# Performance work log

Hardware: AMD Instinct MI355X
Metric: run time of the kernel (lower is better)

## Reference

```python
import jax, jax.numpy as jnp
import numpy as np

EPS = 1e-5  # torch BatchNorm2d default eps

def _bn(x, gamma, beta):
    # training-mode batch statistics over (N,H,W), per channel (biased variance)
    mean = jnp.mean(x, axis=(0, 2, 3), keepdims=True)
    var = jnp.var(x, axis=(0, 2, 3), keepdims=True)
    return gamma[None, :, None, None] * (x - mean) * jax.lax.rsqrt(var + EPS) + beta[None, :, None, None]

def _conv1x1(x, w, b):
    # (B,C,H,W) x (O,C) -> (B,O,H,W)
    return jnp.einsum('bchw,oc->bohw', x, w) + b[None, :, None, None]

def _maxpool2(x):
    B, C, H, W = x.shape
    return x.reshape(B, C, H // 2, 2, W // 2, 2).max(axis=(3, 5))

def setup_inputs() -> dict:
    key = jax.random.key(0)
    ks = jax.random.split(key, 5)
    B, C, H, W = 16, 256, 56, 56
    Ci, Cg = C // 8, C // 4
    def kaiming(k, o, i):
        return jax.random.normal(k, (o, i), jnp.float32) * np.float32(np.sqrt(2.0 / i))
    return {
        'x': jax.random.normal(ks[0], (B, C, H, W), jnp.float32),
        'bn1_gamma': jnp.ones((C,), jnp.float32),
        'bn1_beta': jnp.zeros((C,), jnp.float32),
        'w_g': kaiming(ks[1], Cg, C), 'b_g': jnp.zeros((Cg,), jnp.float32),
        'w_theta': kaiming(ks[2], Ci, C), 'b_theta': jnp.zeros((Ci,), jnp.float32),
        'w_phi': kaiming(ks[3], Ci, C), 'b_phi': jnp.zeros((Ci,), jnp.float32),
        'bn2_gamma': jnp.ones((Cg,), jnp.float32),
        'bn2_beta': jnp.zeros((Cg,), jnp.float32),
        'w_z': kaiming(ks[4], C, Cg), 'b_z': jnp.zeros((C,), jnp.float32),
    }

def reference(x, bn1_gamma, bn1_beta, w_g, b_g, w_theta, b_theta, w_phi, b_phi, bn2_gamma, bn2_beta, w_z, b_z):
    identity = x
    B, C, H, W = x.shape
    xa = jax.nn.relu(_bn(x, bn1_gamma, bn1_beta))
    g_x = _maxpool2(_conv1x1(xa, w_g, b_g))        # (B,Cg,H/2,W/2)
    phi_x = _maxpool2(_conv1x1(xa, w_phi, b_phi))  # (B,Ci,H/2,W/2)
    theta_x = _conv1x1(xa, w_theta, b_theta)       # (B,Ci,H,W)
    Cg = g_x.shape[1]
    Ci = theta_x.shape[1]
    Np = g_x.shape[2] * g_x.shape[3]               # subsampled positions (H/2*W/2)
    g_x = g_x.reshape(B, Cg, Np).transpose(0, 2, 1)      # (B,Np,Cg)
    phi_x = phi_x.reshape(B, Ci, Np)                     # (B,Ci,Np)
    theta_x = theta_x.reshape(B, Ci, H * W).transpose(0, 2, 1)  # (B,HW,Ci)
    f_div_C = jnp.einsum('bnc,bcm->bnm', theta_x, phi_x) / Np   # (B,HW,Np)
    y = jnp.einsum('bnm,bmc->bnc', f_div_C, g_x)                # (B,HW,Cg)
    y = y.transpose(0, 2, 1).reshape(B, Cg, H, W)
    w_y = _conv1x1(jax.nn.relu(_bn(y, bn2_gamma, bn2_beta)), w_z, b_z)
    return w_y + identity
```

## Files before the change

### kernel.cpp

```cpp
#include <hip/hip_runtime.h>
#include <hip/hip_bf16.h>

#define BB 16
#define CC 256
#define HWN 3136
#define NCG 64
#define NCI 32
#define NPP 784

typedef __attribute__((ext_vector_type(8))) short short8;
typedef __attribute__((ext_vector_type(4))) float floatx4;

__device__ __forceinline__ unsigned short f2bf(float f) {
    union { __hip_bfloat16 h; unsigned short u; } cv;
    cv.h = __float2bfloat16(f);
    return cv.u;
}
__device__ __forceinline__ float bf2f(unsigned short u) {
    return __uint_as_float(((unsigned)u) << 16);
}

__global__ __launch_bounds__(256) void k_head(const float* __restrict__ x,
                                              const float* __restrict__ w_t,
                                              const float* __restrict__ w_p,
                                              const float* __restrict__ w_g,
                                              const float* __restrict__ w_z,
                                              unsigned short* __restrict__ wcat,
                                              unsigned short* __restrict__ wzb,
                                              unsigned short* __restrict__ pool,
                                              float* __restrict__ zacc,
                                              float* __restrict__ bn1part) {
    int blk = blockIdx.x;
    int c = threadIdx.x;
    if (blk < 128) {
        int o = blk;
        const float* src = (o < 32) ? (w_t + o * CC)
                          : (o < 64) ? (w_p + (o - 32) * CC)
                                     : (w_g + (o - 64) * CC);
        wcat[o * CC + c] = f2bf(src[c]);
        {
            int r = o * 2 + (c >> 7);
            int kk = c & 127;
            if (kk < 72)
                wzb[r * 72 + kk] = (kk < 64) ? f2bf(w_z[r * 64 + kk]) : (unsigned short)0;
        }
        if (o < 96) {
            int b = c >> 4, kk = c & 15;
            pool[((size_t)(b * 96 + o)) * 800 + 784 + kk] = 0;
        }
        int idx = o * 256 + c;
        if (idx < 17024) zacc[idx] = 0.f;
        return;
    }
    int bc = blk - 128;
    const float4* p = (const float4*)(x + (size_t)bc * HWN);
    int tid = c;
    float s = 0.f, q = 0.f;
    for (int i = tid; i < 784; i += 256) {
        float4 v = p[i];
        s += v.x + v.y + v.z + v.w;
        q += v.x * v.x + v.y * v.y + v.z * v.z + v.w * v.w;
    }
    #pragma unroll
    for (int off = 32; off > 0; off >>= 1) {
        s += __shfl_down(s, off);
        q += __shfl_down(q, off);
    }
    __shared__ float sh[16];
    int wid = tid >> 6, lane = tid & 63;
    if (lane == 0) { sh[wid] = s; sh[8 + wid] = q; }
    __syncthreads();
    if (tid == 0) bn1part[bc]        = sh[0] + sh[1] + sh[2] + sh[3];
    if (tid == 1) bn1part[4096 + bc] = sh[8] + sh[9] + sh[10] + sh[11];
}

__global__ __launch_bounds__(256) void k_conv1(const float* __restrict__ x,
                                               const unsigned short* __restrict__ wcat,
                                               const float* __restrict__ bn1part,
                                               const float* __restrict__ gamma,
                                               const float* __restrict__ beta,
                                               const float* __restrict__ b_g,
                                               const float* __restrict__ b_t,
                                               const float* __restrict__ b_p,
                                               unsigned short* __restrict__ th,
                                               unsigned short* __restrict__ pool,
                                               float* __restrict__ T1g,
                                               float* __restrict__ Gg) {
    int b  = blockIdx.y;
    int bx = blockIdx.x;
    int hw0 = bx * 112;
    int tid = threadIdx.x;
    int wv = tid >> 6, ln = tid & 63;
    int col = ln & 15, quad = ln >> 4;

    __shared__ unsigned short smem[128 * 120];
    unsigned short* As = smem;
    unsigned short* Bs = smem + 4096;
    __shared__ float ab_s[512];
    __shared__ float bias_s[128];

    {
        const float inv = 1.0f / (BB * HWN);
        float s = 0.f, q = 0.f;
        #pragma unroll
        for (int b2 = 0; b2 < BB; ++b2) {
            s += bn1part[b2 * 256 + tid];
            q += bn1part[4096 + b2 * 256 + tid];
        }
        float mean = s * inv;
        float var  = q * inv - mean * mean;
        float a = gamma[tid] * rsqrtf(var + 1e-5f);
        ab_s[tid] = a;
        ab_s[CC + tid] = beta[tid] - mean * a;
    }
    if (tid < 128) {
        int o = tid;
        bias_s[o] = (o < 32) ? b_t[o] : (o < 64) ? b_p[o - 32] : b_g[o - 64];
    }
    __syncthreads();

    floatx4 acc[2][7];
    #pragma unroll
    for (int mt = 0; mt < 2; ++mt)
        for (int nt = 0; nt < 7; ++nt)
            acc[mt][nt] = (floatx4){0.f, 0.f, 0.f, 0.f};

    int p   = tid & 15;
    int hwq = tid >> 4;
    const float* xb = x + (size_t)(b * CC) * HWN + hw0;
    bool q1 = (hwq + 16) < 28;

    float4 pv0[2], pv1[2];
    {
        int c0 = 2 * p;
        pv0[0] = *(const float4*)(xb + (size_t)c0 * HWN + hwq * 4);
        pv1[0] = *(const float4*)(xb + (size_t)(c0 + 1) * HWN + hwq * 4);
        if (q1) {
            pv0[1] = *(const float4*)(xb + (size_t)c0 * HWN + (hwq + 16) * 4);
            pv1[1] = *(const float4*)(xb + (size_t)(c0 + 1) * HWN + (hwq + 16) * 4);
        }
    }

    for (int k0 = 0; k0 < CC; k0 += 32) {
        #pragma unroll
        for (int i = 0; i < 2; ++i) {
            int row = wv * 32 + i * 16 + (ln >> 2);
            int q   = ln & 3;
            const unsigned short* gp = wcat + row * CC + k0 + q * 8;
            __builtin_amdgcn_global_load_lds(
                (const __attribute__((address_space(1))) unsigned int*)gp,
                (__attribute__((address_space(3))) unsigned int*)&As[(wv * 2 + i) * 512],
                16, 0, 0);
        }
        {
            int c0 = k0 + 2 * p;
            float a0 = ab_s[c0],     d0 = ab_s[CC + c0];
            float a1 = ab_s[c0 + 1], d1 = ab_s[CC + c0 + 1];
            unsigned int* bw = (unsigned int*)Bs;
            #pragma unroll
            for (int t = 0; t < 2; ++t) {
                if (t == 0 || q1) {
                    int qi = hwq + 16 * t;
                    float4 v0 = pv0[t], v1 = pv1[t];
                    float r0[4] = { fmaxf(fmaf(a0, v0.x, d0), 0.f), fmaxf(fmaf(a0, v0.y, d0), 0.f),
                                    fmaxf(fmaf(a0, v0.z, d0), 0.f), fmaxf(fmaf(a0, v0.w, d0), 0.f) };
                    float r1[4] = { fmaxf(fmaf(a1, v1.x, d1), 0.f), fmaxf(fmaf(a1, v1.y, d1), 0.f),
                                    fmaxf(fmaf(a1, v1.z, d1), 0.f), fmaxf(fmaf(a1, v1.w, d1), 0.f) };
                    #pragma unroll
                    for (int i = 0; i < 4; ++i) {
                        unsigned int w = (unsigned int)f2bf(r0[i]) | ((unsigned int)f2bf(r1[i]) << 16);
                        bw[(qi * 4 + i) * 16 + p] = w;
                    }
                }
            }
        }
        __syncthreads();

        if (k0 + 32 < CC) {
            int c0 = k0 + 32 + 2 * p;
            pv0[0] = *(const float4*)(xb + (size_t)c0 * HWN + hwq * 4);
            pv1[0] = *(const float4*)(xb + (size_t)(c0 + 1) * HWN + hwq * 4);
            if (q1) {
                pv0[1] = *(const float4*)(xb + (size_t)c0 * HWN + (hwq + 16) * 4);
                pv1[1] = *(const float4*)(xb + (size_t)(c0 + 1) * HWN + (hwq + 16) * 4);
            }
        }

        short8 af0 = *(const short8*)&As[(wv * 32 +      col) * 32 + quad * 8];
        short8 af1 = *(const short8*)&As[(wv * 32 + 16 + col) * 32 + quad * 8];
        #pragma unroll
        for (int nt = 0; nt < 7; ++nt) {
            short8 bf = *(const short8*)&Bs[(nt * 16 + col) * 32 + quad * 8];
            acc[0][nt] = __builtin_amdgcn_mfma_f32_16x16x32_bf16(af0, bf, acc[0][nt], 0, 0, 0);
            acc[1][nt] = __builtin_amdgcn_mfma_f32_16x16x32_bf16(af1, bf, acc[1][nt], 0, 0, 0);
        }
        __syncthreads();
    }

    unsigned short* Ct = smem;
    #pragma unroll
    for (int mt = 0; mt < 2; ++mt) {
        int obase = wv * 32 + mt * 16 + quad * 4;
        #pragma unroll
        for (int r = 0; r < 4; ++r) {
            float bias = bias_s[obase + r];
            #pragma unroll
            for (int nt = 0; nt < 7; ++nt)
                Ct[(obase + r) * 120 + nt * 16 + col] = f2bf(acc[mt][nt][r] + bias);
        }
    }
    __syncthreads();

    #pragma unroll
    for (int i = 0; i < 4; ++i) {
        int e = tid + i * 256;
        if (e < 896) {
            int ch = e / 28, c4 = e - ch * 28;
            ushort4 v = *(const ushort4*)&Ct[ch * 120 + c4 * 4];
            *(ushort4*)&th[((size_t)(b * NCI + ch)) * HWN + hw0 + c4 * 4] = v;
        }
    }
    {
        int row = tid >> 3;
        int seg = tid & 7;
        float s = 0.f;
        #pragma unroll
        for (int j = 0; j < 14; ++j) s += bf2f(Ct[row * 120 + seg * 14 + j]);
        s += __shfl_down(s, 4);
        s += __shfl_down(s, 2);
        s += __shfl_down(s, 1);
        if (seg == 0) atomicAdd(&T1g[b * NCI + row], s);
    }
    {
        int m = wv >> 1, n = wv & 1;
        floatx4 g = (floatx4){0.f, 0.f, 0.f, 0.f};
        short8 z8 = (short8){0, 0, 0, 0, 0, 0, 0, 0};
        #pragma unroll
        for (int ks = 0; ks < 4; ++ks) {
            short8 ga, gb;
            if (ks < 3 || quad < 2) {
                ga = *(const short8*)&Ct[(m * 16 + col) * 120 + ks * 32 + quad * 8];
                gb = *(const short8*)&Ct[(n * 16 + col) * 120 + ks * 32 + quad * 8];
            } else {
                ga = z8; gb = z8;
            }
            g = __builtin_amdgcn_mfma_f32_16x16x32_bf16(ga, gb, g, 0, 0, 0);
        }
        float* gg = Gg + b * 1024 + (m * 16 + quad * 4) * 32 + n * 16 + col;
        #pragma unroll
        for (int r = 0; r < 4; ++r) atomicAdd(&gg[r * 32], g[r]);
    }
    #pragma unroll
    for (int i = 0; i < 11; ++i) {
        int e = tid + i * 256;
        if (e < 2688) {
            int ch = e / 28, m = e - ch * 28;
            const unsigned short* r0p = &Ct[(32 + ch) * 120 + 2 * m];
            float v = fmaxf(fmaxf(bf2f(r0p[0]), bf2f(r0p[1])),
                            fmaxf(bf2f(r0p[56]), bf2f(r0p[57])));
            pool[((size_t)(b * 96 + ch)) * 800 + bx * 28 + m] = f2bf(v);
        }
    }
}

__global__ __launch_bounds__(512) void k_sgemm(const unsigned short* __restrict__ pool,
                                               const float* __restrict__ T1g,
                                               const float* __restrict__ Gg,
                                               unsigned short* __restrict__ Sg,
                                               float* __restrict__ bn2acc) {
    int b = blockIdx.x;
    int tid = threadIdx.x;
    int wv = tid >> 6, ln = tid & 63;
    int col = ln & 15, quad = ln >> 4;
    __shared__ float Sred[8 * 2048];
    __shared__ float Gred[1024];
    __shared__ float T1s[32];
    __shared__ float shs[64], shq[64];

    if (tid < 64) { shs[tid] = 0.f; shq[tid] = 0.f; }
    if (tid < 32) T1s[tid] = T1g[b * NCI + tid];
    for (int idx = tid; idx < 1024; idx += 512) Gred[idx] = Gg[b * 1024 + idx];

    const unsigned short* gbase = pool + ((size_t)(b * 96 + 32)) * 800;
    const unsigned short* pbase = pool + ((size_t)(b * 96)) * 800;
    floatx4 acc[4][2];
    #pragma unroll
    for (int mt = 0; mt < 4; ++mt)
        for (int nt = 0; nt < 2; ++nt)
            acc[mt][nt] = (floatx4){0.f, 0.f, 0.f, 0.f};
    for (int s = wv; s < 25; s += 8) {
        int k0 = s * 32;
        short8 af[4], bfr[2];
        #pragma unroll
        for (int mt = 0; mt < 4; ++mt)
            af[mt] = *(const short8*)&gbase[(mt * 16 + col) * 800 + k0 + quad * 8];
        #pragma unroll
        for (int nt = 0; nt < 2; ++nt)
            bfr[nt] = *(const short8*)&pbase[(nt * 16 + col) * 800 + k0 + quad * 8];
        #pragma unroll
        for (int mt = 0; mt < 4; ++mt)
            #pragma unroll
            for (int nt = 0; nt < 2; ++nt)
                acc[mt][nt] = __builtin_amdgcn_mfma_f32_16x16x32_bf16(af[mt], bfr[nt], acc[mt][nt], 0, 0, 0);
    }
    #pragma unroll
    for (int mt = 0; mt < 4; ++mt)
        for (int nt = 0; nt < 2; ++nt)
            for (int r = 0; r < 4; ++r) {
                int cg = mt * 16 + quad * 4 + r;
                int ci = nt * 16 + col;
                Sred[wv * 2048 + cg * 32 + ci] = acc[mt][nt][r];
            }
    __syncthreads();

    for (int idx = tid; idx < 2048; idx += 512) {
        float s = 0.f;
        #pragma unroll
        for (int w = 0; w < 8; ++w) s += Sred[w * 2048 + idx];
        int cg = idx >> 5, ci = idx & 31;
        unsigned short h = f2bf(s * (1.0f / NPP));
        Sg[(size_t)b * 2560 + cg * 40 + ci] = h;
        Sred[idx] = bf2f(h);
    }
    __syncthreads();

    {
        int cg = tid & 63, part = tid >> 6;
        float sum = 0.f, sq = 0.f;
        #pragma unroll
        for (int i = 0; i < 4; ++i) {
            int ci = part * 4 + i;
            float sv = Sred[cg * 32 + ci];
            sum += sv * T1s[ci];
            float t = 0.f;
            #pragma unroll
            for (int cj = 0; cj < 32; ++cj)
                t += Gred[ci * 32 + cj] * Sred[cg * 32 + cj];
            sq += sv * t;
        }
        atomicAdd(&shs[cg], sum);
        atomicAdd(&shq[cg], sq);
    }
    __syncthreads();
    if (tid < 64) {
        atomicAdd(&bn2acc[tid], shs[tid]);
        atomicAdd(&bn2acc[64 + tid], shq[tid]);
    }
}

__global__ __launch_bounds__(256) void k_convz(const unsigned short* __restrict__ th,
                                               const unsigned short* __restrict__ Sg,
                                               const unsigned short* __restrict__ wzb,
                                               const float* __restrict__ bn2acc,
                                               const float* __restrict__ gamma,
                                               const float* __restrict__ beta,
                                               const float* __restrict__ b_z,
                                               const float* __restrict__ x,
                                               float* __restrict__ out) {
    int b = blockIdx.y;
    int hw0 = blockIdx.x * 64;
    int tid = threadIdx.x;
    int wv = tid >> 6, ln = tid & 63;
    int col = ln & 15, quad = ln >> 4;

    __shared__ unsigned short Wl[256 * 72];
    __shared__ unsigned short TS[5120];
    __shared__ float ab2_s[128];
    unsigned short* Tt = TS;
    unsigned short* St = TS + 2560;
    unsigned short* Yt = TS;

    for (int j = wv; j < 36; j += 4) {
        const unsigned short* gp = wzb + j * 512 + ln * 8;
        __builtin_amdgcn_global_load_lds(
            (const __attribute__((address_space(1))) unsigned int*)gp,
            (__attribute__((address_space(3))) unsigned int*)&Wl[j * 512],
            16, 0, 0);
    }
    if (tid < 64) {
        const float inv = 1.0f / (BB * HWN);
        float mean = bn2acc[tid] * inv;
        float var  = bn2acc[64 + tid] * inv - mean * mean;
        float a = gamma[tid] * rsqrtf(var + 1e-5f);
        ab2_s[tid] = a;
        ab2_s[64 + tid] = beta[tid] - mean * a;
    }
    {
        const unsigned int* sgw = (const unsigned int*)(Sg + (size_t)b * 2560);
        unsigned int* stw = (unsigned int*)St;
        for (int i = tid; i < 1280; i += 256) stw[i] = sgw[i];
    }
    {
        int p2 = tid & 15, hwq = tid >> 4;
        int c0 = 2 * p2;
        const unsigned short* tb = th + (size_t)(b * NCI) * HWN + hw0 + hwq * 4;
        ushort4 v0 = *(const ushort4*)(tb + (size_t)c0 * HWN);
        ushort4 v1 = *(const ushort4*)(tb + (size_t)(c0 + 1) * HWN);
        unsigned int* tw = (unsigned int*)Tt;
        tw[(hwq * 4 + 0) * 20 + p2] = (unsigned)v0.x | ((unsigned)v1.x << 16);
        tw[(hwq * 4 + 1) * 20 + p2] = (unsigned)v0.y | ((unsigned)v1.y << 16);
        tw[(hwq * 4 + 2) * 20 + p2] = (unsigned)v0.z | ((unsigned)v1.z << 16);
        tw[(hwq * 4 + 3) * 20 + p2] = (unsigned)v0.w | ((unsigned)v1.w << 16);
    }
    __syncthreads();

    short8 afy = *(const short8*)&Tt[(wv * 16 + col) * 40 + quad * 8];
    floatx4 yacc[4];
    #pragma unroll
    for (int nt = 0; nt < 4; ++nt) {
        short8 bf = *(const short8*)&St[(nt * 16 + col) * 40 + quad * 8];
        floatx4 z = (floatx4){0.f, 0.f, 0.f, 0.f};
        yacc[nt] = __builtin_amdgcn_mfma_f32_16x16x32_bf16(afy, bf, z, 0, 0, 0);
    }
    __syncthreads();

    #pragma unroll
    for (int nt = 0; nt < 4; ++nt) {
        int cg = nt * 16 + col;
        float a = ab2_s[cg], d = ab2_s[64 + cg];
        #pragma unroll
        for (int r = 0; r < 4; ++r) {
            int hwl = wv * 16 + quad * 4 + r;
            Yt[hwl * 72 + cg] = f2bf(fmaxf(fmaf(a, yacc[nt][r], d), 0.f));
        }
    }
    __syncthreads();

    floatx4 acc[16];
    #pragma unroll
    for (int nt = 0; nt < 16; ++nt) acc[nt] = (floatx4){0.f, 0.f, 0.f, 0.f};

    #pragma unroll
    for (int kk = 0; kk < 2; ++kk) {
        short8 afm = *(const short8*)&Yt[(wv * 16 + col) * 72 + kk * 32 + quad * 8];
        #pragma unroll
        for (int nt = 0; nt < 16; ++nt) {
            short8 bf = *(const short8*)&Wl[(nt * 16 + col) * 72 + kk * 32 + quad * 8];
            acc[nt] = __builtin_amdgcn_mfma_f32_16x16x32_bf16(afm, bf, acc[nt], 0, 0, 0);
        }
    }

    #pragma unroll
    for (int nt = 0; nt < 16; ++nt) {
        int co = nt * 16 + col;
        size_t base = ((size_t)(b * CC + co)) * HWN + hw0 + wv * 16 + quad * 4;
        float4 xv = *(const float4*)&x[base];
        float bz = b_z[co];
        float4 r = make_float4(acc[nt][0] + bz + xv.x, acc[nt][1] + bz + xv.y,
                               acc[nt][2] + bz + xv.z, acc[nt][3] + bz + xv.w);
        *(float4*)&out[base] = r;
    }
}

extern "C" void kernel_launch(void* const* d_in, const int* in_sizes, int n_in,
                              void* d_out, int out_size, void* d_ws, size_t ws_size,
                              hipStream_t stream) {
    (void)in_sizes; (void)n_in; (void)out_size; (void)ws_size;
    const float* x   = (const float*)d_in[0];
    const float* g1  = (const float*)d_in[1];
    const float* b1  = (const float*)d_in[2];
    const float* w_g = (const float*)d_in[3];
    const float* b_g = (const float*)d_in[4];
    const float* w_t = (const float*)d_in[5];
    const float* b_t = (const float*)d_in[6];
    const float* w_p = (const float*)d_in[7];
    const float* b_p = (const float*)d_in[8];
    const float* g2  = (const float*)d_in[9];
    const float* b2  = (const float*)d_in[10];
    const float* w_z = (const float*)d_in[11];
    const float* b_z = (const float*)d_in[12];
    float* out = (float*)d_out;

    float* ws      = (float*)d_ws;
    float* bn1part = ws;
    float* zacc    = ws + 8192;
    float* bn2acc  = ws + 8192;
    float* T1g     = ws + 8320;
    float* Gg      = ws + 8832;
    unsigned short* wcat = (unsigned short*)(ws + 25216);
    unsigned short* wzb  = (unsigned short*)(ws + 41600);
    unsigned short* th   = (unsigned short*)(ws + 50816);
    unsigned short* pool = (unsigned short*)(ws + 853632);
    unsigned short* Sg   = (unsigned short*)(ws + 1468032);

    k_head  <<<dim3(4224),     dim3(256), 0, stream>>>(x, w_t, w_p, w_g, w_z, wcat, wzb, pool, zacc, bn1part);
    k_conv1 <<<dim3(28, BB),   dim3(256), 0, stream>>>(x, wcat, bn1part, g1, b1, b_g, b_t, b_p, th, pool, T1g, Gg);
    k_sgemm <<<dim3(BB),       dim3(512), 0, stream>>>(pool, T1g, Gg, Sg, bn2acc);
    k_convz <<<dim3(49, BB),   dim3(256), 0, stream>>>(th, Sg, wzb, bn2acc, g2, b2, b_z, x, out);
}
```

Measured before the change: 170.5 us.

## Widen conv1 blocks to 512 threads and split sgemm across Cg quarters

k_conv1 now runs 8 waves per block, each owning 16 output rows, with one float4 pair of x per thread instead of two. This cuts per-thread accumulators and registers and raises wave-level parallelism. k_sgemm is split into 4 blocks per batch (one per 16-channel group of g), giving 64 blocks instead of 16 and a smaller reduction buffer. The cost is redundant loads of the phi tiles across blocks and more atomics into bn2acc.

```diff
diff --git a/kernel.cpp b/kernel.cpp
--- a/kernel.cpp
+++ b/kernel.cpp
@@ -4,7 +4,6 @@
 #define BB 16
 #define CC 256
 #define HWN 3136
-#define NCG 64
 #define NCI 32
 #define NPP 784
 
@@ -18,6 +17,20 @@
 }
 __device__ __forceinline__ float bf2f(unsigned short u) {
     return __uint_as_float(((unsigned)u) << 16);
+}
+
+__device__ __forceinline__ void stage_Tt(unsigned short* Tt, const unsigned short* th,
+                                         int b, int hw0, int tid) {
+    int p2 = tid & 15, hwq = tid >> 4;
+    int c0 = 2 * p2;
+    const unsigned short* tb = th + (size_t)(b * NCI) * HWN + hw0 + hwq * 4;
+    ushort4 v0 = *(const ushort4*)(tb + (size_t)c0 * HWN);
+    ushort4 v1 = *(const ushort4*)(tb + (size_t)(c0 + 1) * HWN);
+    unsigned int* tw = (unsigned int*)Tt;
+    tw[(hwq * 4 + 0) * 20 + p2] = (unsigned)v0.x | ((unsigned)v1.x << 16);
+    tw[(hwq * 4 + 1) * 20 + p2] = (unsigned)v0.y | ((unsigned)v1.y << 16);
+    tw[(hwq * 4 + 2) * 20 + p2] = (unsigned)v0.z | ((unsigned)v1.z << 16);
+    tw[(hwq * 4 + 3) * 20 + p2] = (unsigned)v0.w | ((unsigned)v1.w << 16);
 }
 
 __global__ __launch_bounds__(256) void k_head(const float* __restrict__ x,
@@ -74,7 +87,7 @@
     if (tid == 1) bn1part[4096 + bc] = sh[8] + sh[9] + sh[10] + sh[11];
 }
 
-__global__ __launch_bounds__(256) void k_conv1(const float* __restrict__ x,
+__global__ __launch_bounds__(512) void k_conv1(const float* __restrict__ x,
                                                const unsigned short* __restrict__ wcat,
                                                const float* __restrict__ bn1part,
                                                const float* __restrict__ gamma,
@@ -99,7 +112,7 @@
     __shared__ float ab_s[512];
     __shared__ float bias_s[128];
 
-    {
+    if (tid < 256) {
         const float inv = 1.0f / (BB * HWN);
         float s = 0.f, q = 0.f;
         #pragma unroll
@@ -119,101 +132,79 @@
     }
     __syncthreads();
 
-    floatx4 acc[2][7];
-    #pragma unroll
-    for (int mt = 0; mt < 2; ++mt)
-        for (int nt = 0; nt < 7; ++nt)
-            acc[mt][nt] = (floatx4){0.f, 0.f, 0.f, 0.f};
+    floatx4 acc[7];
+    #pragma unroll
+    for (int nt = 0; nt < 7; ++nt)
+        acc[nt] = (floatx4){0.f, 0.f, 0.f, 0.f};
 
     int p   = tid & 15;
     int hwq = tid >> 4;
+    bool act = hwq < 28;
     const float* xb = x + (size_t)(b * CC) * HWN + hw0;
-    bool q1 = (hwq + 16) < 28;
-
-    float4 pv0[2], pv1[2];
-    {
+
+    float4 pv0, pv1;
+    if (act) {
         int c0 = 2 * p;
-        pv0[0] = *(const float4*)(xb + (size_t)c0 * HWN + hwq * 4);
-        pv1[0] = *(const float4*)(xb + (size_t)(c0 + 1) * HWN + hwq * 4);
-        if (q1) {
-            pv0[1] = *(const float4*)(xb + (size_t)c0 * HWN + (hwq + 16) * 4);
-            pv1[1] = *(const float4*)(xb + (size_t)(c0 + 1) * HWN + (hwq + 16) * 4);
-        }
+        pv0 = *(const float4*)(xb + (size_t)c0 * HWN + hwq * 4);
+        pv1 = *(const float4*)(xb + (size_t)(c0 + 1) * HWN + hwq * 4);
     }
 
     for (int k0 = 0; k0 < CC; k0 += 32) {
-        #pragma unroll
-        for (int i = 0; i < 2; ++i) {
-            int row = wv * 32 + i * 16 + (ln >> 2);
-            int q   = ln & 3;
-            const unsigned short* gp = wcat + row * CC + k0 + q * 8;
+        {
+            const unsigned short* gp = wcat + (wv * 16 + (ln >> 2)) * CC + k0 + (ln & 3) * 8;
             __builtin_amdgcn_global_load_lds(
                 (const __attribute__((address_space(1))) unsigned int*)gp,
-                (__attribute__((address_space(3))) unsigned int*)&As[(wv * 2 + i) * 512],
+                (__attribute__((address_space(3))) unsigned int*)&As[wv * 512],
                 16, 0, 0);
         }
-        {
+        if (act) {
             int c0 = k0 + 2 * p;
             float a0 = ab_s[c0],     d0 = ab_s[CC + c0];
             float a1 = ab_s[c0 + 1], d1 = ab_s[CC + c0 + 1];
             unsigned int* bw = (unsigned int*)Bs;
+            float r0[4] = { fmaxf(fmaf(a0, pv0.x, d0), 0.f), fmaxf(fmaf(a0, pv0.y, d0), 0.f),
+                            fmaxf(fmaf(a0, pv0.z, d0), 0.f), fmaxf(fmaf(a0, pv0.w, d0), 0.f) };
+            float r1[4] = { fmaxf(fmaf(a1, pv1.x, d1), 0.f), fmaxf(fmaf(a1, pv1.y, d1), 0.f),
+                            fmaxf(fmaf(a1, pv1.z, d1), 0.f), fmaxf(fmaf(a1, pv1.w, d1), 0.f) };
             #pragma unroll
-            for (int t = 0; t < 2; ++t) {
-                if (t == 0 || q1) {
-                    int qi = hwq + 16 * t;
-                    float4 v0 = pv0[t], v1 = pv1[t];
-                    float r0[4] = { fmaxf(fmaf(a0, v0.x, d0), 0.f), fmaxf(fmaf(a0, v0.y, d0), 0.f),
-                                    fmaxf(fmaf(a0, v0.z, d0), 0.f), fmaxf(fmaf(a0, v0.w, d0), 0.f) };
-                    float r1[4] = { fmaxf(fmaf(a1, v1.x, d1), 0.f), fmaxf(fmaf(a1, v1.y, d1), 0.f),
-                                    fmaxf(fmaf(a1, v1.z, d1), 0.f), fmaxf(fmaf(a1, v1.w, d1), 0.f) };
-                    #pragma unroll
-                    for (int i = 0; i < 4; ++i) {
-                        unsigned int w = (unsigned int)f2bf(r0[i]) | ((unsigned int)f2bf(r1[i]) << 16);
-                        bw[(qi * 4 + i) * 16 + p] = w;
-                    }
-                }
+            for (int i = 0; i < 4; ++i) {
+                unsigned int w = (unsigned int)f2bf(r0[i]) | ((unsigned int)f2bf(r1[i]) << 16);
+                bw[(hwq * 4 + i) * 16 + p] = w;
             }
         }
         __syncthreads();
 
-        if (k0 + 32 < CC) {
+        if (act && k0 + 32 < CC) {
             int c0 = k0 + 32 + 2 * p;
-            pv0[0] = *(const float4*)(xb + (size_t)c0 * HWN + hwq * 4);
-            pv1[0] = *(const float4*)(xb + (size_t)(c0 + 1) * HWN + hwq * 4);
-            if (q1) {
-                pv0[1] = *(const float4*)(xb + (size_t)c0 * HWN + (hwq + 16) * 4);
-                pv1[1] = *(const float4*)(xb + (size_t)(c0 + 1) * HWN + (hwq + 16) * 4);
-            }
-        }
-
-        short8 af0 = *(const short8*)&As[(wv * 32 +      col) * 32 + quad * 8];
-        short8 af1 = *(const short8*)&As[(wv * 32 + 16 + col) * 32 + quad * 8];
+            pv0 = *(const float4*)(xb + (size_t)c0 * HWN + hwq * 4);
+            pv1 = *(const float4*)(xb + (size_t)(c0 + 1) * HWN + hwq * 4);
+        }
+
+        short8 af = *(const short8*)&As[(wv * 16 + col) * 32 + quad * 8];
         #pragma unroll
         for (int nt = 0; nt < 7; ++nt) {
             short8 bf = *(const short8*)&Bs[(nt * 16 + col) * 32 + quad * 8];
-            acc[0][nt] = __builtin_amdgcn_mfma_f32_16x16x32_bf16(af0, bf, acc[0][nt], 0, 0, 0);
-            acc[1][nt] = __builtin_amdgcn_mfma_f32_16x16x32_bf16(af1, bf, acc[1][nt], 0, 0, 0);
+            acc[nt] = __builtin_amdgcn_mfma_f32_16x16x32_bf16(af, bf, acc[nt], 0, 0, 0);
         }
         __syncthreads();
     }
 
     unsigned short* Ct = smem;
-    #pragma unroll
-    for (int mt = 0; mt < 2; ++mt) {
-        int obase = wv * 32 + mt * 16 + quad * 4;
+    {
+        int obase = wv * 16 + quad * 4;
         #pragma unroll
         for (int r = 0; r < 4; ++r) {
             float bias = bias_s[obase + r];
             #pragma unroll
             for (int nt = 0; nt < 7; ++nt)
-                Ct[(obase + r) * 120 + nt * 16 + col] = f2bf(acc[mt][nt][r] + bias);
-        }
-    }
-    __syncthreads();
-
-    #pragma unroll
-    for (int i = 0; i < 4; ++i) {
-        int e = tid + i * 256;
+                Ct[(obase + r) * 120 + nt * 16 + col] = f2bf(acc[nt][r] + bias);
+        }
+    }
+    __syncthreads();
+
+    #pragma unroll
+    for (int i = 0; i < 2; ++i) {
+        int e = tid + i * 512;
         if (e < 896) {
             int ch = e / 28, c4 = e - ch * 28;
             ushort4 v = *(const ushort4*)&Ct[ch * 120 + c4 * 4];
@@ -221,22 +212,25 @@
         }
     }
     {
-        int row = tid >> 3;
-        int seg = tid & 7;
+        int row = tid >> 4;
+        int seg = tid & 15;
         float s = 0.f;
         #pragma unroll
-        for (int j = 0; j < 14; ++j) s += bf2f(Ct[row * 120 + seg * 14 + j]);
+        for (int j = 0; j < 7; ++j) s += bf2f(Ct[row * 120 + seg * 7 + j]);
+        s += __shfl_down(s, 8);
         s += __shfl_down(s, 4);
         s += __shfl_down(s, 2);
         s += __shfl_down(s, 1);
         if (seg == 0) atomicAdd(&T1g[b * NCI + row], s);
     }
     {
-        int m = wv >> 1, n = wv & 1;
+        int m = (wv >> 1) & 1, n = wv & 1;
+        int ks0 = (wv >> 2) * 2;
         floatx4 g = (floatx4){0.f, 0.f, 0.f, 0.f};
         short8 z8 = (short8){0, 0, 0, 0, 0, 0, 0, 0};
         #pragma unroll
-        for (int ks = 0; ks < 4; ++ks) {
+        for (int kx = 0; kx < 2; ++kx) {
+            int ks = ks0 + kx;
             short8 ga, gb;
             if (ks < 3 || quad < 2) {
                 ga = *(const short8*)&Ct[(m * 16 + col) * 120 + ks * 32 + quad * 8];
@@ -246,13 +240,13 @@
             }
             g = __builtin_amdgcn_mfma_f32_16x16x32_bf16(ga, gb, g, 0, 0, 0);
         }
-        float* gg = Gg + b * 1024 + (m * 16 + quad * 4) * 32 + n * 16 + col;
-        #pragma unroll
-        for (int r = 0; r < 4; ++r) atomicAdd(&gg[r * 32], g[r]);
-    }
-    #pragma unroll
-    for (int i = 0; i < 11; ++i) {
-        int e = tid + i * 256;
+        float* ggp = Gg + b * 1024 + (m * 16 + quad * 4) * 32 + n * 16 + col;
+        #pragma unroll
+        for (int r = 0; r < 4; ++r) atomicAdd(&ggp[r * 32], g[r]);
+    }
+    #pragma unroll
+    for (int i = 0; i < 6; ++i) {
+        int e = tid + i * 512;
         if (e < 2688) {
             int ch = e / 28, m = e - ch * 28;
             const unsigned short* r0p = &Ct[(32 + ch) * 120 + 2 * m];
@@ -263,88 +257,75 @@
     }
 }
 
-__global__ __launch_bounds__(512) void k_sgemm(const unsigned short* __restrict__ pool,
+__global__ __launch_bounds__(256) void k_sgemm(const unsigned short* __restrict__ pool,
                                                const float* __restrict__ T1g,
                                                const float* __restrict__ Gg,
                                                unsigned short* __restrict__ Sg,
                                                float* __restrict__ bn2acc) {
-    int b = blockIdx.x;
+    int q = blockIdx.x;
+    int b = blockIdx.y;
     int tid = threadIdx.x;
     int wv = tid >> 6, ln = tid & 63;
     int col = ln & 15, quad = ln >> 4;
-    __shared__ float Sred[8 * 2048];
+    __shared__ float Sred[4 * 512];
     __shared__ float Gred[1024];
     __shared__ float T1s[32];
-    __shared__ float shs[64], shq[64];
-
-    if (tid < 64) { shs[tid] = 0.f; shq[tid] = 0.f; }
+    __shared__ float shs[16], shq[16];
+
+    if (tid < 16) { shs[tid] = 0.f; shq[tid] = 0.f; }
     if (tid < 32) T1s[tid] = T1g[b * NCI + tid];
-    for (int idx = tid; idx < 1024; idx += 512) Gred[idx] = Gg[b * 1024 + idx];
-
-    const unsigned short* gbase = pool + ((size_t)(b * 96 + 32)) * 800;
+    for (int idx = tid; idx < 1024; idx += 256) Gred[idx] = Gg[b * 1024 + idx];
+
+    const unsigned short* gbase = pool + ((size_t)(b * 96 + 32 + q * 16)) * 800;
     const unsigned short* pbase = pool + ((size_t)(b * 96)) * 800;
-    floatx4 acc[4][2];
-    #pragma unroll
-    for (int mt = 0; mt < 4; ++mt)
-        for (int nt = 0; nt < 2; ++nt)
-            acc[mt][nt] = (floatx4){0.f, 0.f, 0.f, 0.f};
-    for (int s = wv; s < 25; s += 8) {
-        int k0 = s * 32;
-        short8 af[4], bfr[2];
-        #pragma unroll
-        for (int mt = 0; mt < 4; ++mt)
-            af[mt] = *(const short8*)&gbase[(mt * 16 + col) * 800 + k0 + quad * 8];
-        #pragma unroll
-        for (int nt = 0; nt < 2; ++nt)
-            bfr[nt] = *(const short8*)&pbase[(nt * 16 + col) * 800 + k0 + quad * 8];
-        #pragma unroll
-        for (int mt = 0; mt < 4; ++mt)
-            #pragma unroll
-            for (int nt = 0; nt < 2; ++nt)
-                acc[mt][nt] = __builtin_amdgcn_mfma_f32_16x16x32_bf16(af[mt], bfr[nt], acc[mt][nt], 0, 0, 0);
-    }
-    #pragma unroll
-    for (int mt = 0; mt < 4; ++mt)
-        for (int nt = 0; nt < 2; ++nt)
-            for (int r = 0; r < 4; ++r) {
-                int cg = mt * 16 + quad * 4 + r;
-                int ci = nt * 16 + col;
-                Sred[wv * 2048 + cg * 32 + ci] = acc[mt][nt][r];
-            }
-    __syncthreads();
-
-    for (int idx = tid; idx < 2048; idx += 512) {
-        float s = 0.f;
-        #pragma unroll
-        for (int w = 0; w < 8; ++w) s += Sred[w * 2048 + idx];
-        int cg = idx >> 5, ci = idx & 31;
+    floatx4 acc[2];
+    acc[0] = (floatx4){0.f, 0.f, 0.f, 0.f};
+    acc[1] = (floatx4){0.f, 0.f, 0.f, 0.f};
+    for (int ks = wv; ks < 25; ks += 4) {
+        int k0 = ks * 32;
+        short8 af = *(const short8*)&gbase[(size_t)col * 800 + k0 + quad * 8];
+        #pragma unroll
+        for (int nt = 0; nt < 2; ++nt) {
+            short8 bf = *(const short8*)&pbase[(nt * 16 + col) * 800 + k0 + quad * 8];
+            acc[nt] = __builtin_amdgcn_mfma_f32_16x16x32_bf16(af, bf, acc[nt], 0, 0, 0);
+        }
+    }
+    #pragma unroll
+    for (int nt = 0; nt < 2; ++nt)
+        for (int r = 0; r < 4; ++r)
+            Sred[wv * 512 + (quad * 4 + r) * 32 + nt * 16 + col] = acc[nt][r];
+    __syncthreads();
+
+    for (int idx = tid; idx < 512; idx += 256) {
+        float s = Sred[idx] + Sred[512 + idx] + Sred[1024 + idx] + Sred[1536 + idx];
+        int cgl = idx >> 5, ci = idx & 31;
         unsigned short h = f2bf(s * (1.0f / NPP));
-        Sg[(size_t)b * 2560 + cg * 40 + ci] = h;
+        Sg[(size_t)b * 2560 + (q * 16 + cgl) * 40 + ci] = h;
         Sred[idx] = bf2f(h);
     }
     __syncthreads();
 
     {
-        int cg = tid & 63, part = tid >> 6;
+        int cgl = tid & 15, part = tid >> 4;
         float sum = 0.f, sq = 0.f;
         #pragma unroll
-        for (int i = 0; i < 4; ++i) {
-            int ci = part * 4 + i;
-            float sv = Sred[cg * 32 + ci];
+        for (int i = 0; i < 2; ++i) {
+            int ci = part * 2 + i;
+            float sv = Sred[cgl * 32 + ci];
             sum += sv * T1s[ci];
-            float t = 0.f;
+            float t2 = 0.f;
             #pragma unroll
             for (int cj = 0; cj < 32; ++cj)
-                t += Gred[ci * 32 + cj] * Sred[cg * 32 + cj];
-            sq += sv * t;
-        }
-        atomicAdd(&shs[cg], sum);
-        atomicAdd(&shq[cg], sq);
-    }
-    __syncthreads();
-    if (tid < 64) {
-        atomicAdd(&bn2acc[tid], shs[tid]);
-        atomicAdd(&bn2acc[64 + tid], shq[tid]);
+                t2 += Gred[ci * 32 + cj] * Sred[cgl * 32 + cj];
+            sq += sv * t2;
+        }
+        atomicAdd(&shs[cgl], sum);
+        atomicAdd(&shq[cgl], sq);
+    }
+    __syncthreads();
+    if (tid < 16) {
+        atomicAdd(&bn2acc[q * 16 + tid], shs[tid]);
+        atomicAdd(&bn2acc[64 + q * 16 + tid], shq[tid]);
     }
 }
 
@@ -390,18 +371,7 @@
         unsigned int* stw = (unsigned int*)St;
         for (int i = tid; i < 1280; i += 256) stw[i] = sgw[i];
     }
-    {
-        int p2 = tid & 15, hwq = tid >> 4;
-        int c0 = 2 * p2;
-        const unsigned short* tb = th + (size_t)(b * NCI) * HWN + hw0 + hwq * 4;
-        ushort4 v0 = *(const ushort4*)(tb + (size_t)c0 * HWN);
-        ushort4 v1 = *(const ushort4*)(tb + (size_t)(c0 + 1) * HWN);
-        unsigned int* tw = (unsigned int*)Tt;
-        tw[(hwq * 4 + 0) * 20 + p2] = (unsigned)v0.x | ((unsigned)v1.x << 16);
-        tw[(hwq * 4 + 1) * 20 + p2] = (unsigned)v0.y | ((unsigned)v1.y << 16);
-        tw[(hwq * 4 + 2) * 20 + p2] = (unsigned)v0.z | ((unsigned)v1.z << 16);
-        tw[(hwq * 4 + 3) * 20 + p2] = (unsigned)v0.w | ((unsigned)v1.w << 16);
-    }
+    stage_Tt(Tt, th, b, hw0, tid);
     __syncthreads();
 
     short8 afy = *(const short8*)&Tt[(wv * 16 + col) * 40 + quad * 8];
@@ -484,7 +454,7 @@
     unsigned short* Sg   = (unsigned short*)(ws + 1468032);
 
     k_head  <<<dim3(4224),     dim3(256), 0, stream>>>(x, w_t, w_p, w_g, w_z, wcat, wzb, pool, zacc, bn1part);
-    k_conv1 <<<dim3(28, BB),   dim3(256), 0, stream>>>(x, wcat, bn1part, g1, b1, b_g, b_t, b_p, th, pool, T1g, Gg);
-    k_sgemm <<<dim3(BB),       dim3(512), 0, stream>>>(pool, T1g, Gg, Sg, bn2acc);
+    k_conv1 <<<dim3(28, BB),   dim3(512), 0, stream>>>(x, wcat, bn1part, g1, b1, b_g, b_t, b_p, th, pool, T1g, Gg);
+    k_sgemm <<<dim3(4, BB),    dim3(256), 0, stream>>>(pool, T1g, Gg, Sg, bn2acc);
     k_convz <<<dim3(49, BB),   dim3(256), 0, stream>>>(th, Sg, wzb, bn2acc, g2, b2, b_z, x, out);
 }
```

Result: no change. 170.1 us (-0.2%).
